# Kernel tuning notes

Hardware: AMD Instinct MI355X
Metric: run time of the kernel (lower is better)

## Reference

```python
import jax, jax.numpy as jnp
import numpy as np

N = 20000      # nodes
E = 320000     # edges (before self loops)
D_IN = 256
D_H = 256
D_E = 8
NEG_SLOPE = 0.2


def setup_inputs() -> dict:
    key = jax.random.key(0)
    ks = jax.random.split(key, 12)
    x = jax.random.normal(ks[0], (N, D_IN), jnp.float32)
    edge_index = jax.random.randint(ks[1], (2, E), 0, N, dtype=jnp.int32)
    edge_attr = jax.random.normal(ks[2], (E, D_E), jnp.float32)
    batch = jnp.zeros((N,), jnp.int32)

    def gat_params(k, d_in):
        k1, k2, k3 = jax.random.split(k, 3)
        W = jax.random.normal(k1, (d_in, D_H), jnp.float32) * (1.0 / np.sqrt(d_in))
        a_s = jax.random.normal(k2, (D_H,), jnp.float32) * 0.1
        a_d = jax.random.normal(k3, (D_H,), jnp.float32) * 0.1
        b = jnp.zeros((D_H,), jnp.float32)
        return W, a_s, a_d, b

    W1, as1, ad1, b1 = gat_params(ks[3], D_IN)
    W2, as2, ad2, b2 = gat_params(ks[4], D_H)
    W3, as3, ad3, b3 = gat_params(ks[5], D_H)
    return dict(x=x, edge_index=edge_index, edge_attr=edge_attr, batch=batch,
                W1=W1, as1=as1, ad1=ad1, b1=b1,
                W2=W2, as2=as2, ad2=ad2, b2=b2,
                W3=W3, as3=as3, ad3=ad3, b3=b3)


def gat_conv(x, src, dst, W, a_src, a_dst, b):
    # PyG GATConv, heads=1: h = x W; alpha_e = leakyrelu(<h_src,a_s> + <h_dst,a_d>)
    h = x @ W                                  # [N, D_H]
    s = h @ a_src                              # [N]
    d = h @ a_dst                              # [N]
    alpha = jax.nn.leaky_relu(s[src] + d[dst], NEG_SLOPE)   # [Etot]
    n = h.shape[0]
    m = jax.ops.segment_max(alpha, dst, num_segments=n)     # per-dst max
    ex = jnp.exp(alpha - m[dst])
    denom = jax.ops.segment_sum(ex, dst, num_segments=n)
    w = ex / (denom[dst] + 1e-16)
    out = jax.ops.segment_sum(h[src] * w[:, None], dst, num_segments=n)
    return out + b


def reference(x, edge_index, edge_attr, batch,
              W1, as1, ad1, b1, W2, as2, ad2, b2, W3, as3, ad3, b3):
    # row-normalize input features (zero norms -> 1e-8)
    norms = jnp.linalg.norm(x, axis=1, keepdims=True)
    norms = jnp.where(norms == 0, 1e-8, norms)
    x = x / norms

    # add self loops once (GATConv default add_self_loops=True);
    # edge_attr is ignored since edge_dim=None in GATConv defaults.
    loop = jnp.arange(N, dtype=edge_index.dtype)
    src = jnp.concatenate([edge_index[0], loop])
    dst = jnp.concatenate([edge_index[1], loop])

    x = jax.nn.gelu(gat_conv(x, src, dst, W1, as1, ad1, b1), approximate=False)
    x = jax.nn.gelu(gat_conv(x, src, dst, W2, as2, ad2, b2), approximate=False)
    x = jax.nn.gelu(gat_conv(x, src, dst, W3, as3, ad3, b3), approximate=False)
    return x
```

## Files before the change

### kernel.cpp

```cpp
#include <hip/hip_runtime.h>
#include <math.h>

#define NN 20000
#define EE 320000
#define DD 256
#define ETOT (EE + NN)

typedef __attribute__((ext_vector_type(8))) short bf8;
typedef __attribute__((ext_vector_type(4))) float f32x4;

__device__ __forceinline__ float gelu_exact(float x) {
    return 0.5f * x * (1.0f + erff(x * 0.70710678118654752f));
}

__device__ __forceinline__ unsigned short f2bf(float v) {
    unsigned u = __float_as_uint(v);
    u += 0x7fffu + ((u >> 16) & 1u);
    return (unsigned short)(u >> 16);
}
__device__ __forceinline__ float bf2f(unsigned short h) {
    return __uint_as_float(((unsigned)h) << 16);
}
__device__ __forceinline__ void split2(float v, unsigned short& hi, unsigned short& lo) {
    hi = f2bf(v);
    lo = f2bf(v - bf2f(hi));
}

__global__ __launch_bounds__(256) void norm_k(const float* __restrict__ X,
                                              unsigned short* __restrict__ Xh,
                                              unsigned short* __restrict__ Xl) {
    int wave = (blockIdx.x * 256 + threadIdx.x) >> 6;
    int lane = threadIdx.x & 63;
    const float4 v = *(const float4*)&X[wave * DD + lane * 4];
    float ss = v.x * v.x + v.y * v.y + v.z * v.z + v.w * v.w;
    for (int off = 32; off > 0; off >>= 1) ss += __shfl_down(ss, off, 64);
    ss = __shfl(ss, 0, 64);
    float n = sqrtf(ss);
    if (n == 0.0f) n = 1e-8f;
    float inv = 1.0f / n;
    float o[4] = {v.x * inv, v.y * inv, v.z * inv, v.w * inv};
    ushort4 hv, lv;
    split2(o[0], hv.x, lv.x);
    split2(o[1], hv.y, lv.y);
    split2(o[2], hv.z, lv.z);
    split2(o[3], hv.w, lv.w);
    *(ushort4*)&Xh[wave * DD + lane * 4] = hv;
    *(ushort4*)&Xl[wave * DD + lane * 4] = lv;
}

__global__ __launch_bounds__(256) void splitw_k(const float* __restrict__ W,
                                                unsigned short* __restrict__ Wht,
                                                unsigned short* __restrict__ Wlt) {
    __shared__ float tile[64][65];
    int t = threadIdx.x;
    int k0 = blockIdx.x * 64;
    int c0 = blockIdx.y * 64;
#pragma unroll
    for (int i = 0; i < 16; ++i) {
        int idx = t + i * 256;
        int r = idx >> 6, c = idx & 63;
        tile[r][c] = W[(k0 + r) * DD + c0 + c];
    }
    __syncthreads();
#pragma unroll
    for (int i = 0; i < 16; ++i) {
        int idx = t + i * 256;
        int r = idx >> 6, c = idx & 63;
        float v = tile[c][r];
        unsigned short hi, lo;
        split2(v, hi, lo);
        Wht[(c0 + r) * DD + k0 + c] = hi;
        Wlt[(c0 + r) * DD + k0 + c] = lo;
    }
}

__global__ void initdeg_k(int* deg) {
    int i = blockIdx.x * 256 + threadIdx.x;
    if (i < NN) deg[i] = 1;
}

__global__ void count_k(const int* __restrict__ ei, int* deg) {
    int e = blockIdx.x * 256 + threadIdx.x;
    if (e < EE) atomicAdd(&deg[ei[EE + e]], 1);
}

#define SCAN_T 1024
#define ITEMS 20
__global__ __launch_bounds__(SCAN_T) void scan_k(const int* __restrict__ deg, int* __restrict__ offs,
                                                 int* __restrict__ cursor) {
    __shared__ int part[SCAN_T];
    int t = threadIdx.x;
    int base = t * ITEMS;
    int local[ITEMS];
    int sum = 0;
#pragma unroll
    for (int i = 0; i < ITEMS; ++i) {
        int idx = base + i;
        int v = (idx < NN) ? deg[idx] : 0;
        local[i] = v;
        sum += v;
    }
    part[t] = sum;
    __syncthreads();
    for (int s = 1; s < SCAN_T; s <<= 1) {
        int v = (t >= s) ? part[t - s] : 0;
        __syncthreads();
        part[t] += v;
        __syncthreads();
    }
    int run = (t == 0) ? 0 : part[t - 1];
#pragma unroll
    for (int i = 0; i < ITEMS; ++i) {
        int idx = base + i;
        if (idx < NN) {
            offs[idx] = run;
            cursor[idx] = run;
            run += local[i];
        }
    }
    if (t == SCAN_T - 1) offs[NN] = part[SCAN_T - 1];
}

__global__ void fill_k(const int* __restrict__ ei, int* cursor, int* __restrict__ csr) {
    int e = blockIdx.x * 256 + threadIdx.x;
    if (e < EE) {
        int s = ei[e];
        int d = ei[EE + e];
        int p = atomicAdd(&cursor[d], 1);
        csr[p] = s;
    } else if (e < EE + NN) {
        int i = e - EE;
        int p = atomicAdd(&cursor[i], 1);
        csr[p] = i;
    }
}

#define LDB 40
__global__ __launch_bounds__(256) void gemm_mfma(const unsigned short* __restrict__ Xh,
                                                 const unsigned short* __restrict__ Xl,
                                                 const unsigned short* __restrict__ Bh,
                                                 const unsigned short* __restrict__ Bl,
                                                 float* __restrict__ H) {
    __shared__ unsigned short sBh[128 * LDB], sBl[128 * LDB];
    int t = threadIdx.x;
    int m0 = blockIdx.x * 64;
    int n0 = blockIdx.y * 128;
    int w = t >> 6, l = t & 63;
    int rofs = l & 15, kch = l >> 4;

    f32x4 acc[8] = {};

    int c1 = t, c2 = t + 256;
    int br1 = c1 >> 2, bo1 = (c1 & 3) * 8;
    int br2 = c2 >> 2, bo2 = (c2 & 3) * 8;
    const unsigned short* Bh1 = &Bh[(n0 + br1) * DD + bo1];
    const unsigned short* Bh2 = &Bh[(n0 + br2) * DD + bo2];
    const unsigned short* Bl1 = &Bl[(n0 + br1) * DD + bo1];
    const unsigned short* Bl2 = &Bl[(n0 + br2) * DD + bo2];
    bf8 rbh1 = *(const bf8*)Bh1;
    bf8 rbh2 = *(const bf8*)Bh2;
    bf8 rbl1 = *(const bf8*)Bl1;
    bf8 rbl2 = *(const bf8*)Bl2;

    int arow = m0 + w * 16 + rofs;
    bool aval = arow < NN;
    const unsigned short* Ahp = &Xh[(size_t)arow * DD + kch * 8];
    const unsigned short* Alp = &Xl[(size_t)arow * DD + kch * 8];
    bf8 zero = {0, 0, 0, 0, 0, 0, 0, 0};
    bf8 ah = aval ? *(const bf8*)Ahp : zero;
    bf8 al = aval ? *(const bf8*)Alp : zero;

    for (int k0 = 0; k0 < DD; k0 += 32) {
        if (k0) __syncthreads();
        *(bf8*)&sBh[br1 * LDB + bo1] = rbh1;
        *(bf8*)&sBh[br2 * LDB + bo2] = rbh2;
        *(bf8*)&sBl[br1 * LDB + bo1] = rbl1;
        *(bf8*)&sBl[br2 * LDB + bo2] = rbl2;
        __syncthreads();
        int kn = k0 + 32;
        bf8 nah = zero, nal = zero;
        if (kn < DD) {
            rbh1 = *(const bf8*)(Bh1 + kn);
            rbh2 = *(const bf8*)(Bh2 + kn);
            rbl1 = *(const bf8*)(Bl1 + kn);
            rbl2 = *(const bf8*)(Bl2 + kn);
            if (aval) {
                nah = *(const bf8*)(Ahp + kn);
                nal = *(const bf8*)(Alp + kn);
            }
        }
#pragma unroll
        for (int nt = 0; nt < 8; ++nt) {
            int r = nt * 16 + rofs;
            bf8 bh = *(const bf8*)&sBh[r * LDB + kch * 8];
            bf8 bl = *(const bf8*)&sBl[r * LDB + kch * 8];
            acc[nt] = __builtin_amdgcn_mfma_f32_16x16x32_bf16(ah, bh, acc[nt], 0, 0, 0);
            acc[nt] = __builtin_amdgcn_mfma_f32_16x16x32_bf16(ah, bl, acc[nt], 0, 0, 0);
            acc[nt] = __builtin_amdgcn_mfma_f32_16x16x32_bf16(al, bh, acc[nt], 0, 0, 0);
        }
        ah = nah;
        al = nal;
    }
    int row0 = m0 + w * 16 + (l >> 4) * 4;
    int colb = l & 15;
#pragma unroll
    for (int nt = 0; nt < 8; ++nt) {
        int cc = n0 + nt * 16 + colb;
#pragma unroll
        for (int r = 0; r < 4; ++r) {
            int row = row0 + r;
            if (row < NN) H[(size_t)row * DD + cc] = acc[nt][r];
        }
    }
}

__global__ __launch_bounds__(256) void sd_k(const float* __restrict__ H, const float* __restrict__ a_s,
                                            const float* __restrict__ a_d, float* __restrict__ sArr,
                                            float* __restrict__ dArr) {
    int wave = (blockIdx.x * 256 + threadIdx.x) >> 6;
    int lane = threadIdx.x & 63;
    const float4 h = *(const float4*)&H[wave * DD + lane * 4];
    const float4 vs = *(const float4*)&a_s[lane * 4];
    const float4 vd = *(const float4*)&a_d[lane * 4];
    float s = h.x * vs.x + h.y * vs.y + h.z * vs.z + h.w * vs.w;
    float d = h.x * vd.x + h.y * vd.y + h.z * vd.z + h.w * vd.w;
    for (int off = 32; off > 0; off >>= 1) {
        s += __shfl_down(s, off, 64);
        d += __shfl_down(d, off, 64);
    }
    if (lane == 0) {
        sArr[wave] = s;
        dArr[wave] = d;
    }
}

__global__ __launch_bounds__(256) void wnorm_k(const float* __restrict__ sArr, const float* __restrict__ dArr,
                                               const int* __restrict__ offs, const int* __restrict__ csr,
                                               float* __restrict__ wn) {
    int dst = (blockIdx.x * 256 + threadIdx.x) >> 6;
    int lane = threadIdx.x & 63;
    int beg = offs[dst], end = offs[dst + 1];
    float dd = dArr[dst];
    float den = 0.0f;
    for (int base = beg; base < end; base += 64) {
        int idx = base + lane;
        float w = 0.0f;
        if (idx < end) {
            float a = sArr[csr[idx]] + dd;
            a = (a > 0.0f) ? a : 0.2f * a;
            w = expf(a);
            wn[idx] = w;
        }
        den += w;
    }
    for (int off = 32; off > 0; off >>= 1) den += __shfl_down(den, off, 64);
    den = __shfl(den, 0, 64);
    float inv = 1.0f / den;
    for (int base = beg; base < end; base += 64) {
        int idx = base + lane;
        if (idx < end) wn[idx] *= inv;
    }
}

__global__ __launch_bounds__(256) void spmm_k(const float* __restrict__ H, const float* __restrict__ wn,
                                              const int* __restrict__ offs, const int* __restrict__ csr,
                                              const float* __restrict__ bias,
                                              unsigned short* __restrict__ Oh,
                                              unsigned short* __restrict__ Ol,
                                              float* __restrict__ outf32) {
    int t = threadIdx.x;
    int sub = t & 7;
    int dst = blockIdx.y * 32 + (t >> 3);
    int dim = blockIdx.x * 32 + sub * 4;

    int beg = offs[dst], end = offs[dst + 1];
    const float* Hs = H + dim;

    float4 A0 = make_float4(0, 0, 0, 0), A1 = A0, A2 = A0, A3 = A0;

    int e = beg;
    for (; e + 3 < end; e += 4) {
        int s0 = csr[e], s1 = csr[e + 1], s2 = csr[e + 2], s3 = csr[e + 3];
        float w0 = wn[e], w1 = wn[e + 1], w2 = wn[e + 2], w3 = wn[e + 3];
        const float4 h0 = *(const float4*)&Hs[(size_t)s0 * DD];
        const float4 h1 = *(const float4*)&Hs[(size_t)s1 * DD];
        const float4 h2 = *(const float4*)&Hs[(size_t)s2 * DD];
        const float4 h3 = *(const float4*)&Hs[(size_t)s3 * DD];
        A0.x += w0 * h0.x; A0.y += w0 * h0.y; A0.z += w0 * h0.z; A0.w += w0 * h0.w;
        A1.x += w1 * h1.x; A1.y += w1 * h1.y; A1.z += w1 * h1.z; A1.w += w1 * h1.w;
        A2.x += w2 * h2.x; A2.y += w2 * h2.y; A2.z += w2 * h2.z; A2.w += w2 * h2.w;
        A3.x += w3 * h3.x; A3.y += w3 * h3.y; A3.z += w3 * h3.z; A3.w += w3 * h3.w;
    }
    for (; e < end; ++e) {
        int s0 = csr[e];
        float w0 = wn[e];
        const float4 h0 = *(const float4*)&Hs[(size_t)s0 * DD];
        A0.x += w0 * h0.x; A0.y += w0 * h0.y; A0.z += w0 * h0.z; A0.w += w0 * h0.w;
    }

    const float4 b = *(const float4*)&bias[dim];
    float o0 = gelu_exact(A0.x + A1.x + A2.x + A3.x + b.x);
    float o1 = gelu_exact(A0.y + A1.y + A2.y + A3.y + b.y);
    float o2 = gelu_exact(A0.z + A1.z + A2.z + A3.z + b.z);
    float o3 = gelu_exact(A0.w + A1.w + A2.w + A3.w + b.w);

    ushort4 hv, lv;
    split2(o0, hv.x, lv.x);
    split2(o1, hv.y, lv.y);
    split2(o2, hv.z, lv.z);
    split2(o3, hv.w, lv.w);
    *(ushort4*)&Oh[dst * DD + dim] = hv;
    *(ushort4*)&Ol[dst * DD + dim] = lv;
    if (outf32) {
        float4 o = make_float4(o0, o1, o2, o3);
        *(float4*)&outf32[dst * DD + dim] = o;
    }
}

extern "C" void kernel_launch(void* const* d_in, const int* in_sizes, int n_in,
                              void* d_out, int out_size, void* d_ws, size_t ws_size,
                              hipStream_t stream) {
    const float* x  = (const float*)d_in[0];
    const int* ei   = (const int*)d_in[1];
    const float* W1 = (const float*)d_in[4];
    const float* as1 = (const float*)d_in[5];
    const float* ad1 = (const float*)d_in[6];
    const float* b1 = (const float*)d_in[7];
    const float* W2 = (const float*)d_in[8];
    const float* as2 = (const float*)d_in[9];
    const float* ad2 = (const float*)d_in[10];
    const float* b2 = (const float*)d_in[11];
    const float* W3 = (const float*)d_in[12];
    const float* as3 = (const float*)d_in[13];
    const float* ad3 = (const float*)d_in[14];
    const float* b3 = (const float*)d_in[15];

    float* H = (float*)d_ws;
    unsigned short* Xh = (unsigned short*)(H + (size_t)NN * DD);
    unsigned short* Xl = Xh + (size_t)NN * DD;
    unsigned short* Wht1 = Xl + (size_t)NN * DD;
    unsigned short* Wlt1 = Wht1 + DD * DD;
    unsigned short* Wht2 = Wlt1 + DD * DD;
    unsigned short* Wlt2 = Wht2 + DD * DD;
    unsigned short* Wht3 = Wlt2 + DD * DD;
    unsigned short* Wlt3 = Wht3 + DD * DD;
    float* sArr = (float*)(Wlt3 + DD * DD);
    float* dArr = sArr + NN;
    int* offs = (int*)(dArr + NN);
    int* cursor = offs + (NN + 1);
    int* csr = cursor + NN;
    int* deg = csr + ETOT;
    float* wn = (float*)(deg + NN);

    initdeg_k<<<(NN + 255) / 256, 256, 0, stream>>>(deg);
    count_k<<<(EE + 255) / 256, 256, 0, stream>>>(ei, deg);
    scan_k<<<1, SCAN_T, 0, stream>>>(deg, offs, cursor);
    fill_k<<<(ETOT + 255) / 256, 256, 0, stream>>>(ei, cursor, csr);

    dim3 wgrid(4, 4);
    splitw_k<<<wgrid, 256, 0, stream>>>(W1, Wht1, Wlt1);
    splitw_k<<<wgrid, 256, 0, stream>>>(W2, Wht2, Wlt2);
    splitw_k<<<wgrid, 256, 0, stream>>>(W3, Wht3, Wlt3);

    norm_k<<<NN / 4, 256, 0, stream>>>(x, Xh, Xl);

    dim3 ggrid((NN + 63) / 64, DD / 128);
    dim3 sgrid(DD / 32, NN / 32);

    gemm_mfma<<<ggrid, 256, 0, stream>>>(Xh, Xl, Wht1, Wlt1, H);
    sd_k<<<NN / 4, 256, 0, stream>>>(H, as1, ad1, sArr, dArr);
    wnorm_k<<<NN / 4, 256, 0, stream>>>(sArr, dArr, offs, csr, wn);
    spmm_k<<<sgrid, 256, 0, stream>>>(H, wn, offs, csr, b1, Xh, Xl, nullptr);

    gemm_mfma<<<ggrid, 256, 0, stream>>>(Xh, Xl, Wht2, Wlt2, H);
    sd_k<<<NN / 4, 256, 0, stream>>>(H, as2, ad2, sArr, dArr);
    wnorm_k<<<NN / 4, 256, 0, stream>>>(sArr, dArr, offs, csr, wn);
    spmm_k<<<sgrid, 256, 0, stream>>>(H, wn, offs, csr, b2, Xh, Xl, nullptr);

    gemm_mfma<<<ggrid, 256, 0, stream>>>(Xh, Xl, Wht3, Wlt3, H);
    sd_k<<<NN / 4, 256, 0, stream>>>(H, as3, ad3, sArr, dArr);
    wnorm_k<<<NN / 4, 256, 0, stream>>>(sArr, dArr, offs, csr, wn);
    spmm_k<<<sgrid, 256, 0, stream>>>(H, wn, offs, csr, b3, Xh, Xl, (float*)d_out);
}
```

Measured before the change: 371.0 us.

## Fuse attention scores into GEMM epilogue and softmax weights into SpMM

The GEMM epilogue now computes the per-node src/dst attention dot products and accumulates them with atomics, which removes the separate sd_k pass over H. The edge softmax normalization moves into spmm_k: weights and source indices are staged in LDS per 32-destination block, so the wnorm_k kernel and the wn global array go away. Self-loop insertion moves into scan_k, deg init and score zeroing fold into norm_k, and the three weight-split launches become one. The cost is float atomics in the GEMM, which make the score sums order-nondeterministic. There is also a fixed EDGE_CAP LDS buffer that overflows if a 32-node block has more than 1536 edges.

```diff
diff --git a/kernel.cpp b/kernel.cpp
--- a/kernel.cpp
+++ b/kernel.cpp
@@ -5,6 +5,7 @@
 #define EE 320000
 #define DD 256
 #define ETOT (EE + NN)
+#define EDGE_CAP 1536
 
 typedef __attribute__((ext_vector_type(8))) short bf8;
 typedef __attribute__((ext_vector_type(4))) float f32x4;
@@ -28,9 +29,16 @@
 
 __global__ __launch_bounds__(256) void norm_k(const float* __restrict__ X,
                                               unsigned short* __restrict__ Xh,
-                                              unsigned short* __restrict__ Xl) {
-    int wave = (blockIdx.x * 256 + threadIdx.x) >> 6;
-    int lane = threadIdx.x & 63;
+                                              unsigned short* __restrict__ Xl,
+                                              float* __restrict__ sdZero,
+                                              int* __restrict__ deg) {
+    int t = threadIdx.x;
+    int bid = blockIdx.x;
+    if (t < 24) sdZero[bid * 24 + t] = 0.0f;
+    if (t >= 32 && t < 36) deg[bid * 4 + (t - 32)] = 1;
+
+    int wave = (bid * 256 + t) >> 6;
+    int lane = t & 63;
     const float4 v = *(const float4*)&X[wave * DD + lane * 4];
     float ss = v.x * v.x + v.y * v.y + v.z * v.z + v.w * v.w;
     for (int off = 32; off > 0; off >>= 1) ss += __shfl_down(ss, off, 64);
@@ -48,13 +56,16 @@
     *(ushort4*)&Xl[wave * DD + lane * 4] = lv;
 }
 
-__global__ __launch_bounds__(256) void splitw_k(const float* __restrict__ W,
-                                                unsigned short* __restrict__ Wht,
-                                                unsigned short* __restrict__ Wlt) {
+__global__ __launch_bounds__(256) void splitw_k(const float* __restrict__ W1, const float* __restrict__ W2,
+                                                const float* __restrict__ W3, unsigned short* __restrict__ Whl) {
     __shared__ float tile[64][65];
     int t = threadIdx.x;
     int k0 = blockIdx.x * 64;
     int c0 = blockIdx.y * 64;
+    int z = blockIdx.z;
+    const float* W = (z == 0) ? W1 : (z == 1) ? W2 : W3;
+    unsigned short* Wht = Whl + (size_t)z * 2 * DD * DD;
+    unsigned short* Wlt = Wht + DD * DD;
 #pragma unroll
     for (int i = 0; i < 16; ++i) {
         int idx = t + i * 256;
@@ -74,11 +85,6 @@
     }
 }
 
-__global__ void initdeg_k(int* deg) {
-    int i = blockIdx.x * 256 + threadIdx.x;
-    if (i < NN) deg[i] = 1;
-}
-
 __global__ void count_k(const int* __restrict__ ei, int* deg) {
     int e = blockIdx.x * 256 + threadIdx.x;
     if (e < EE) atomicAdd(&deg[ei[EE + e]], 1);
@@ -87,7 +93,7 @@
 #define SCAN_T 1024
 #define ITEMS 20
 __global__ __launch_bounds__(SCAN_T) void scan_k(const int* __restrict__ deg, int* __restrict__ offs,
-                                                 int* __restrict__ cursor) {
+                                                 int* __restrict__ cursor, int* __restrict__ csr) {
     __shared__ int part[SCAN_T];
     int t = threadIdx.x;
     int base = t * ITEMS;
@@ -114,7 +120,8 @@
         int idx = base + i;
         if (idx < NN) {
             offs[idx] = run;
-            cursor[idx] = run;
+            cursor[idx] = run + 1;
+            csr[run] = idx;
             run += local[i];
         }
     }
@@ -128,19 +135,19 @@
         int d = ei[EE + e];
         int p = atomicAdd(&cursor[d], 1);
         csr[p] = s;
-    } else if (e < EE + NN) {
-        int i = e - EE;
-        int p = atomicAdd(&cursor[i], 1);
-        csr[p] = i;
     }
 }
 
 #define LDB 40
-__global__ __launch_bounds__(256) void gemm_mfma(const unsigned short* __restrict__ Xh,
-                                                 const unsigned short* __restrict__ Xl,
-                                                 const unsigned short* __restrict__ Bh,
-                                                 const unsigned short* __restrict__ Bl,
-                                                 float* __restrict__ H) {
+__global__ __launch_bounds__(256) void gemm_sd(const unsigned short* __restrict__ Xh,
+                                               const unsigned short* __restrict__ Xl,
+                                               const unsigned short* __restrict__ Bh,
+                                               const unsigned short* __restrict__ Bl,
+                                               const float* __restrict__ a_s,
+                                               const float* __restrict__ a_d,
+                                               float* __restrict__ H,
+                                               float* __restrict__ sArr,
+                                               float* __restrict__ dArr) {
     __shared__ unsigned short sBh[128 * LDB], sBl[128 * LDB];
     int t = threadIdx.x;
     int m0 = blockIdx.x * 64;
@@ -203,85 +210,81 @@
     }
     int row0 = m0 + w * 16 + (l >> 4) * 4;
     int colb = l & 15;
+    float sp[4] = {0, 0, 0, 0}, dp[4] = {0, 0, 0, 0};
 #pragma unroll
     for (int nt = 0; nt < 8; ++nt) {
         int cc = n0 + nt * 16 + colb;
+        float vas = a_s[cc], vad = a_d[cc];
 #pragma unroll
         for (int r = 0; r < 4; ++r) {
             int row = row0 + r;
             if (row < NN) H[(size_t)row * DD + cc] = acc[nt][r];
-        }
-    }
-}
-
-__global__ __launch_bounds__(256) void sd_k(const float* __restrict__ H, const float* __restrict__ a_s,
-                                            const float* __restrict__ a_d, float* __restrict__ sArr,
-                                            float* __restrict__ dArr) {
-    int wave = (blockIdx.x * 256 + threadIdx.x) >> 6;
-    int lane = threadIdx.x & 63;
-    const float4 h = *(const float4*)&H[wave * DD + lane * 4];
-    const float4 vs = *(const float4*)&a_s[lane * 4];
-    const float4 vd = *(const float4*)&a_d[lane * 4];
-    float s = h.x * vs.x + h.y * vs.y + h.z * vs.z + h.w * vs.w;
-    float d = h.x * vd.x + h.y * vd.y + h.z * vd.z + h.w * vd.w;
-    for (int off = 32; off > 0; off >>= 1) {
-        s += __shfl_down(s, off, 64);
-        d += __shfl_down(d, off, 64);
-    }
-    if (lane == 0) {
-        sArr[wave] = s;
-        dArr[wave] = d;
-    }
-}
-
-__global__ __launch_bounds__(256) void wnorm_k(const float* __restrict__ sArr, const float* __restrict__ dArr,
-                                               const int* __restrict__ offs, const int* __restrict__ csr,
-                                               float* __restrict__ wn) {
-    int dst = (blockIdx.x * 256 + threadIdx.x) >> 6;
-    int lane = threadIdx.x & 63;
-    int beg = offs[dst], end = offs[dst + 1];
-    float dd = dArr[dst];
-    float den = 0.0f;
-    for (int base = beg; base < end; base += 64) {
-        int idx = base + lane;
-        float w = 0.0f;
-        if (idx < end) {
-            float a = sArr[csr[idx]] + dd;
-            a = (a > 0.0f) ? a : 0.2f * a;
-            w = expf(a);
-            wn[idx] = w;
-        }
-        den += w;
-    }
-    for (int off = 32; off > 0; off >>= 1) den += __shfl_down(den, off, 64);
-    den = __shfl(den, 0, 64);
-    float inv = 1.0f / den;
-    for (int base = beg; base < end; base += 64) {
-        int idx = base + lane;
-        if (idx < end) wn[idx] *= inv;
-    }
-}
-
-__global__ __launch_bounds__(256) void spmm_k(const float* __restrict__ H, const float* __restrict__ wn,
-                                              const int* __restrict__ offs, const int* __restrict__ csr,
-                                              const float* __restrict__ bias,
+            sp[r] += acc[nt][r] * vas;
+            dp[r] += acc[nt][r] * vad;
+        }
+    }
+#pragma unroll
+    for (int m = 1; m < 16; m <<= 1) {
+#pragma unroll
+        for (int r = 0; r < 4; ++r) {
+            sp[r] += __shfl_xor(sp[r], m, 64);
+            dp[r] += __shfl_xor(dp[r], m, 64);
+        }
+    }
+    if (colb == 0) {
+#pragma unroll
+        for (int r = 0; r < 4; ++r) {
+            int row = row0 + r;
+            if (row < NN) {
+                atomicAdd(&sArr[row], sp[r]);
+                atomicAdd(&dArr[row], dp[r]);
+            }
+        }
+    }
+}
+
+__global__ __launch_bounds__(256) void spmm_k(const float* __restrict__ H, const float* __restrict__ sArr,
+                                              const float* __restrict__ dArr, const int* __restrict__ offs,
+                                              const int* __restrict__ csr, const float* __restrict__ bias,
                                               unsigned short* __restrict__ Oh,
                                               unsigned short* __restrict__ Ol,
                                               float* __restrict__ outf32) {
+    __shared__ float wLds[EDGE_CAP];
+    __shared__ int sLds[EDGE_CAP];
     int t = threadIdx.x;
     int sub = t & 7;
-    int dst = blockIdx.y * 32 + (t >> 3);
+    int g = t >> 3;
+    int dst0 = blockIdx.y * 32;
+    int dst = dst0 + g;
     int dim = blockIdx.x * 32 + sub * 4;
 
+    int blkBeg = offs[dst0];
     int beg = offs[dst], end = offs[dst + 1];
+    float dd = dArr[dst];
+
+    float den = 0.0f;
+    for (int e = beg + sub; e < end; e += 8) {
+        int s = csr[e];
+        float a = sArr[s] + dd;
+        a = (a > 0.0f) ? a : 0.2f * a;
+        float wv = expf(a);
+        wLds[e - blkBeg] = wv;
+        sLds[e - blkBeg] = s;
+        den += wv;
+    }
+    den += __shfl_xor(den, 1, 64);
+    den += __shfl_xor(den, 2, 64);
+    den += __shfl_xor(den, 4, 64);
+    float inv = 1.0f / den;
+    for (int e = beg + sub; e < end; e += 8) wLds[e - blkBeg] *= inv;
+    __syncthreads();
+
     const float* Hs = H + dim;
-
     float4 A0 = make_float4(0, 0, 0, 0), A1 = A0, A2 = A0, A3 = A0;
-
-    int e = beg;
-    for (; e + 3 < end; e += 4) {
-        int s0 = csr[e], s1 = csr[e + 1], s2 = csr[e + 2], s3 = csr[e + 3];
-        float w0 = wn[e], w1 = wn[e + 1], w2 = wn[e + 2], w3 = wn[e + 3];
+    int e = beg - blkBeg, lend = end - blkBeg;
+    for (; e + 3 < lend; e += 4) {
+        int s0 = sLds[e], s1 = sLds[e + 1], s2 = sLds[e + 2], s3 = sLds[e + 3];
+        float w0 = wLds[e], w1 = wLds[e + 1], w2 = wLds[e + 2], w3 = wLds[e + 3];
         const float4 h0 = *(const float4*)&Hs[(size_t)s0 * DD];
         const float4 h1 = *(const float4*)&Hs[(size_t)s1 * DD];
         const float4 h2 = *(const float4*)&Hs[(size_t)s2 * DD];
@@ -291,9 +294,9 @@
         A2.x += w2 * h2.x; A2.y += w2 * h2.y; A2.z += w2 * h2.z; A2.w += w2 * h2.w;
         A3.x += w3 * h3.x; A3.y += w3 * h3.y; A3.z += w3 * h3.z; A3.w += w3 * h3.w;
     }
-    for (; e < end; ++e) {
-        int s0 = csr[e];
-        float w0 = wn[e];
+    for (; e < lend; ++e) {
+        int s0 = sLds[e];
+        float w0 = wLds[e];
         const float4 h0 = *(const float4*)&Hs[(size_t)s0 * DD];
         A0.x += w0 * h0.x; A0.y += w0 * h0.y; A0.z += w0 * h0.z; A0.w += w0 * h0.w;
     }
@@ -338,47 +341,33 @@
     float* H = (float*)d_ws;
     unsigned short* Xh = (unsigned short*)(H + (size_t)NN * DD);
     unsigned short* Xl = Xh + (size_t)NN * DD;
-    unsigned short* Wht1 = Xl + (size_t)NN * DD;
-    unsigned short* Wlt1 = Wht1 + DD * DD;
-    unsigned short* Wht2 = Wlt1 + DD * DD;
-    unsigned short* Wlt2 = Wht2 + DD * DD;
-    unsigned short* Wht3 = Wlt2 + DD * DD;
-    unsigned short* Wlt3 = Wht3 + DD * DD;
-    float* sArr = (float*)(Wlt3 + DD * DD);
-    float* dArr = sArr + NN;
-    int* offs = (int*)(dArr + NN);
+    unsigned short* Whl = Xl + (size_t)NN * DD;
+    float* sd = (float*)(Whl + (size_t)6 * DD * DD);
+    int* offs = (int*)(sd + (size_t)6 * NN);
     int* cursor = offs + (NN + 1);
     int* csr = cursor + NN;
     int* deg = csr + ETOT;
-    float* wn = (float*)(deg + NN);
-
-    initdeg_k<<<(NN + 255) / 256, 256, 0, stream>>>(deg);
+
+    float* sA1 = sd,           *dA1 = sd + NN;
+    float* sA2 = sd + 2 * NN,  *dA2 = sd + 3 * NN;
+    float* sA3 = sd + 4 * NN,  *dA3 = sd + 5 * NN;
+    unsigned short* Wt1 = Whl;
+    unsigned short* Wt2 = Whl + (size_t)2 * DD * DD;
+    unsigned short* Wt3 = Whl + (size_t)4 * DD * DD;
+
+    norm_k<<<NN / 4, 256, 0, stream>>>(x, Xh, Xl, sd, deg);
     count_k<<<(EE + 255) / 256, 256, 0, stream>>>(ei, deg);
-    scan_k<<<1, SCAN_T, 0, stream>>>(deg, offs, cursor);
-    fill_k<<<(ETOT + 255) / 256, 256, 0, stream>>>(ei, cursor, csr);
-
-    dim3 wgrid(4, 4);
-    splitw_k<<<wgrid, 256, 0, stream>>>(W1, Wht1, Wlt1);
-    splitw_k<<<wgrid, 256, 0, stream>>>(W2, Wht2, Wlt2);
-    splitw_k<<<wgrid, 256, 0, stream>>>(W3, Wht3, Wlt3);
-
-    norm_k<<<NN / 4, 256, 0, stream>>>(x, Xh, Xl);
+    scan_k<<<1, SCAN_T, 0, stream>>>(deg, offs, cursor, csr);
+    fill_k<<<(EE + 255) / 256, 256, 0, stream>>>(ei, cursor, csr);
+    splitw_k<<<dim3(4, 4, 3), 256, 0, stream>>>(W1, W2, W3, Whl);
 
     dim3 ggrid((NN + 63) / 64, DD / 128);
     dim3 sgrid(DD / 32, NN / 32);
 
-    gemm_mfma<<<ggrid, 256, 0, stream>>>(Xh, Xl, Wht1, Wlt1, H);
-    sd_k<<<NN / 4, 256, 0, stream>>>(H, as1, ad1, sArr, dArr);
-    wnorm_k<<<NN / 4, 256, 0, stream>>>(sArr, dArr, offs, csr, wn);
-    spmm_k<<<sgrid, 256, 0, stream>>>(H, wn, offs, csr, b1, Xh, Xl, nullptr);
-
-    gemm_mfma<<<ggrid, 256, 0, stream>>>(Xh, Xl, Wht2, Wlt2, H);
-    sd_k<<<NN / 4, 256, 0, stream>>>(H, as2, ad2, sArr, dArr);
-    wnorm_k<<<NN / 4, 256, 0, stream>>>(sArr, dArr, offs, csr, wn);
-    spmm_k<<<sgrid, 256, 0, stream>>>(H, wn, offs, csr, b2, Xh, Xl, nullptr);
-
-    gemm_mfma<<<ggrid, 256, 0, stream>>>(Xh, Xl, Wht3, Wlt3, H);
-    sd_k<<<NN / 4, 256, 0, stream>>>(H, as3, ad3, sArr, dArr);
-    wnorm_k<<<NN / 4, 256, 0, stream>>>(sArr, dArr, offs, csr, wn);
-    spmm_k<<<sgrid, 256, 0, stream>>>(H, wn, offs, csr, b3, Xh, Xl, (float*)d_out);
-}
+    gemm_sd<<<ggrid, 256, 0, stream>>>(Xh, Xl, Wt1, Wt1 + DD * DD, as1, ad1, H, sA1, dA1);
+    spmm_k<<<sgrid, 256, 0, stream>>>(H, sA1, dA1, offs, csr, b1, Xh, Xl, nullptr);
+    gemm_sd<<<ggrid, 256, 0, stream>>>(Xh, Xl, Wt2, Wt2 + DD * DD, as2, ad2, H, sA2, dA2);
+    spmm_k<<<sgrid, 256, 0, stream>>>(H, sA2, dA2, offs, csr, b2, Xh, Xl, nullptr);
+    gemm_sd<<<ggrid, 256, 0, stream>>>(Xh, Xl, Wt3, Wt3 + DD * DD, as3, ad3, H, sA3, dA3);
+    spmm_k<<<sgrid, 256, 0, stream>>>(H, sA3, dA3, offs, csr, b3, Xh, Xl, (float*)d_out);
+}
```

Result: faster. 340.8 us (-8.1%).
